# Optimization experiments

Hardware: AMD Instinct MI355X
Metric: run time of the kernel (lower is better)

Reference implementation:

```python
import jax, jax.numpy as jnp
import numpy as np

B, DIM, N, W, L = 8192, 100, 50, 256, 4  # paths, assets, timesteps, MLP width, n_layers
R = 0.05  # risk-free rate


def _mlp(x, W_in, b_in, W_h, b_h, W_out, b_out):
    # Net: Linear+ReLU, (L-1) hidden Linear+ReLU, final Linear (no activation)
    h = jax.nn.relu(x @ W_in + b_in)
    def body(h, wb):
        Wl, bl = wb
        return jax.nn.relu(h @ Wl + bl), None
    h, _ = jax.lax.scan(body, h, (W_h, b_h))
    return h @ W_out + b_out


def _init_net(key, n_in, n_out):
    ks = jax.random.split(key, 6)
    def lin(k, fi, fo):
        s = 1.0 / np.sqrt(fi)
        return jax.random.uniform(k, (fi, fo), jnp.float32, -s, s)
    W_in = lin(ks[0], n_in, W)
    b_in = jnp.zeros((W,), jnp.float32)
    W_h = jnp.stack([lin(jax.random.fold_in(ks[1], l), W, W) for l in range(L - 1)])
    b_h = jnp.zeros((L - 1, W), jnp.float32)
    W_out = lin(ks[2], W, n_out)
    b_out = jnp.zeros((n_out,), jnp.float32)
    return W_in, b_in, W_h, b_h, W_out, b_out


def setup_inputs() -> dict:
    key = jax.random.key(0)
    k_s0, k_dw, k_g, k_v = jax.random.split(key, 4)
    S0 = jax.random.uniform(k_s0, (B, DIM), jnp.float32, 0.5, 1.5)  # positive prices
    dW = jax.random.normal(k_dw, (N - 1, B, DIM), jnp.float32)  # unscaled increments
    timegrid = jnp.linspace(0.0, 1.0, N).astype(jnp.float32)
    # volatility matrix: rows of cholesky(cov) scaled by sigma_i
    cov = 0.9 * np.eye(DIM) + 0.1 * np.ones((DIM, DIM))
    C = np.linalg.cholesky(cov)
    sigma = 0.2 * np.ones(DIM)
    V = jnp.asarray(sigma[:, None] * C, jnp.float32)
    Wg_in, bg_in, Wg_h, bg_h, Wg_out, bg_out = _init_net(k_g, DIM + 1, DIM)
    Wv_in, bv_in, Wv_h, bv_h, Wv_out, bv_out = _init_net(k_v, DIM + 1, 1)
    return dict(S0=S0, dW=dW, timegrid=timegrid, volatility_mat=V,
                Wg_in=Wg_in, bg_in=bg_in, Wg_h=Wg_h, bg_h=bg_h, Wg_out=Wg_out, bg_out=bg_out,
                Wv_in=Wv_in, bv_in=bv_in, Wv_h=Wv_h, bv_h=bv_h, Wv_out=Wv_out, bv_out=bv_out)


def reference(S0, dW, timegrid, volatility_mat,
              Wg_in, bg_in, Wg_h, bg_h, Wg_out, bg_out,
              Wv_in, bv_in, Wv_h, bv_h, Wv_out, bv_out):
    r = jnp.float32(R)
    dt = timegrid[1:] - timegrid[:-1]                     # [N-1]
    dWs = jnp.sqrt(dt)[:, None, None] * dW                # sqrt(h)*randn, [N-1,B,DIM]
    bsz = S0.shape[0]

    inp0 = jnp.concatenate([jnp.full((bsz, 1), timegrid[0], S0.dtype), S0], axis=1)
    v0 = _mlp(inp0, Wv_in, bv_in, Wv_h, bv_h, Wv_out, bv_out)   # [B,1]

    def step(carry, xs):
        S_old, vOld, error = carry
        tp, tc, h, dWi = xs
        # S_old * (volatility_mat @ dW^T)^T == S_old * (dW @ V^T)
        vol = S_old * (dWi @ volatility_mat.T)                            # [B,DIM]
        inp_g = jnp.concatenate([jnp.full((bsz, 1), tp, S_old.dtype), S_old], axis=1)
        grad = _mlp(inp_g, Wg_in, bg_in, Wg_h, bg_h, Wg_out, bg_out)      # [B,DIM]
        stoch_int = jnp.sum(grad * vol, axis=1, keepdims=True)            # [B,1]
        S_new = S_old + r * S_old * h + vol
        inp_v = jnp.concatenate([jnp.full((bsz, 1), tc, S_new.dtype), S_new], axis=1)
        vNew = _mlp(inp_v, Wv_in, bv_in, Wv_h, bv_h, Wv_out, bv_out)      # [B,1]
        err_i = jax.lax.stop_gradient(vNew) - vOld * (1.0 + r * h) - stoch_int
        return (S_new, vNew, error + err_i ** 2), None

    init = (S0, v0, jnp.zeros_like(v0))
    (S_f, v_f, error), _ = jax.lax.scan(step, init, (timegrid[:-1], timegrid[1:], dt, dWs))
    return v_f, S_f, error
```

## Files before the change

### kernel.cpp

```cpp
#include <hip/hip_runtime.h>
#include <hip/hip_bf16.h>

#define DIMN 100
#define NPATH 8192
#define NT 50
#define HW 256
#define RRATE 0.05f

typedef __hip_bfloat16 bf16;
typedef _Float16 h16;
typedef __attribute__((ext_vector_type(8))) _Float16 h16x8;
typedef __attribute__((ext_vector_type(4))) _Float16 h16x4;
typedef __attribute__((ext_vector_type(4))) float f32x4;

__device__ __forceinline__ float ldin(const void* p, long i, int f32) {
    return f32 ? ((const float*)p)[i] : __bfloat162float(((const bf16*)p)[i]);
}

__global__ void probe_kernel(const void* tgp, int* flag) {
    if (threadIdx.x == 0 && blockIdx.x == 0) {
        const unsigned short* u = (const unsigned short*)tgp;
        *flag = (u[1] == 0) ? 1 : 0;
    }
}

__global__ void init_kernel(const void* S0, float* S_carry,
                            const void* V, float* Vt, const int* dflag) {
    const int f = *dflag;
    const long i = (long)blockIdx.x * blockDim.x + threadIdx.x;
    if (i < (long)NPATH * DIMN) S_carry[i] = ldin(S0, i, f);
    if (i < DIMN * DIMN) {
        const long d = i / DIMN, k = i % DIMN;
        Vt[k * DIMN + d] = ldin(V, d * DIMN + k, f);
    }
}

__global__ void pack_kernel(const void* Wg_in, const void* Wg_h, const void* Wg_out,
                            const void* Wv_in, const void* Wv_h,
                            h16* __restrict__ P, const int* __restrict__ dflag)
{
    const int f = *dflag;
    const long i = (long)blockIdx.x * blockDim.x + threadIdx.x;
    if (i >= 491520) return;
    long j; int NTk, kind; const void* src; long soff = 0;
    if (i < 32768)       { j = i;          NTk = 4; kind = 0; src = Wg_in; }
    else if (i < 229376) { long t = i - 32768;  j = t & 65535; NTk = 8; kind = 1; src = Wg_h;
                           soff = (long)(t >> 16) * 65536; }
    else if (i < 262144) { j = i - 229376; NTk = 8; kind = 2; src = Wg_out; }
    else if (i < 294912) { j = i - 262144; NTk = 4; kind = 0; src = Wv_in; }
    else                 { long t = i - 294912; j = t & 65535; NTk = 8; kind = 1; src = Wv_h;
                           soff = (long)(t >> 16) * 65536; }
    const int tile = (int)(j >> 9), lane = (int)((j >> 3) & 63), e = (int)(j & 7);
    const int tn = tile / NTk, tk = tile - tn * NTk;
    const int n = tn * 16 + (lane & 15);
    const int k = tk * 32 + (lane >> 4) * 8 + e;
    float v;
    if (kind == 0)      v = (k < 101) ? ldin(src, (long)k * 256 + n, f) : 0.f;
    else if (kind == 1) v = ldin(src, soff + (long)k * 256 + n, f);
    else                v = (n < 100) ? ldin(src, (long)k * 100 + n, f) : 0.f;
    P[i] = (h16)v;
}

template <bool A_RAW>
__global__ __launch_bounds__(256)
void gemm_kernel(const void* A, long aOff, int K,
                 const float* __restrict__ Bw, int N,
                 float* __restrict__ Cout, const int* __restrict__ dflag)
{
    const int f = *dflag;
    __shared__ float As[8][128];
    __shared__ float Bs[8][128];
    const int tid = threadIdx.x;
    const int tx = tid & 15, ty = tid >> 4;
    const long rowBase = (long)blockIdx.x * 128;
    const int colBase = blockIdx.y * 128;

    float acc[8][8];
#pragma unroll
    for (int i = 0; i < 8; i++)
#pragma unroll
        for (int j = 0; j < 8; j++) acc[i][j] = 0.f;

    for (int k0 = 0; k0 < K; k0 += 8) {
        {
            const int l = tid * 4;
            const int row = l >> 3;
            const int col = l & 7;
            const long abase = aOff + (rowBase + row) * (long)K + (k0 + col);
#pragma unroll
            for (int q = 0; q < 4; q++)
                As[col + q][row] = (k0 + col + q < K) ? ldin(A, abase + q, f) : 0.f;
        }
#pragma unroll
        for (int q = 0; q < 4; q++) {
            const int l = tid + 256 * q;
            const int kk = l >> 7, col = l & 127;
            const int gk = k0 + kk, gc = colBase + col;
            Bs[kk][col] = (gk < K && gc < N) ? Bw[(long)gk * N + gc] : 0.f;
        }
        __syncthreads();
#pragma unroll
        for (int kk = 0; kk < 8; kk++) {
            float a[8], b[8];
            const float4 a0 = *(const float4*)&As[kk][ty * 8];
            const float4 a1 = *(const float4*)&As[kk][ty * 8 + 4];
            const float4 b0 = *(const float4*)&Bs[kk][tx * 8];
            const float4 b1 = *(const float4*)&Bs[kk][tx * 8 + 4];
            a[0]=a0.x;a[1]=a0.y;a[2]=a0.z;a[3]=a0.w;a[4]=a1.x;a[5]=a1.y;a[6]=a1.z;a[7]=a1.w;
            b[0]=b0.x;b[1]=b0.y;b[2]=b0.z;b[3]=b0.w;b[4]=b1.x;b[5]=b1.y;b[6]=b1.z;b[7]=b1.w;
#pragma unroll
            for (int i = 0; i < 8; i++)
#pragma unroll
                for (int j = 0; j < 8; j++)
                    acc[i][j] += a[i] * b[j];
        }
        __syncthreads();
    }

#pragma unroll
    for (int i = 0; i < 8; i++) {
        const long row = rowBase + ty * 8 + i;
        const int colb = colBase + tx * 8;
        if (colb + 7 < N) {
            float4* cp = (float4*)(Cout + row * (long)N + colb);
            cp[0] = make_float4(acc[i][0], acc[i][1], acc[i][2], acc[i][3]);
            cp[1] = make_float4(acc[i][4], acc[i][5], acc[i][6], acc[i][7]);
        } else {
#pragma unroll
            for (int j = 0; j < 8; j++)
                if (colb + j < N) Cout[row * (long)N + colb + j] = acc[i][j];
        }
    }
}

__global__ __launch_bounds__(256)
void scan_chunk_kernel(float* __restrict__ S_carry, float* __restrict__ D,
                       const void* tgp, h16* __restrict__ Sh,
                       int t0, int Cg, void* outBase, h16* __restrict__ Shf,
                       int writeSf, const int* __restrict__ dflag)
{
    const int f = *dflag;
    const long idx = (long)blockIdx.x * blockDim.x + threadIdx.x;
    if (idx >= (long)NPATH * DIMN) return;
    const long b = idx / DIMN;
    const int d = (int)(idx - b * DIMN);
    float s = S_carry[idx];
    for (int lt = 0; lt < Cg; lt++) {
        const int t = t0 + lt;
        const float h = ldin(tgp, t + 1, f) - ldin(tgp, t, f);
        const long off = (long)lt * (NPATH * DIMN) + idx;
        const float vol = s * D[off] * sqrtf(h);
        const long shr = ((long)lt * NPATH + b) * 104;
        Sh[shr + 1 + d] = (h16)s;
        if (d == 0) Sh[shr] = (h16)ldin(tgp, t, f);
        if (d < 3) Sh[shr + 101 + d] = (h16)0.f;
        D[off] = vol;
        s = s + RRATE * s * h + vol;
    }
    S_carry[idx] = s;
    if (writeSf) {
        if (f) ((float*)outBase)[NPATH + idx] = s;
        else   ((bf16*)outBase)[NPATH + idx] = __float2bfloat16(s);
        Shf[b * 104 + 1 + d] = (h16)s;
        if (d == 0) Shf[b * 104] = (h16)ldin(tgp, NT - 1, f);
        if (d < 3) Shf[b * 104 + 101 + d] = (h16)0.f;
    }
}

template<int NTW>
__device__ __forceinline__ void init_acc(f32x4 acc[2][4], const float* __restrict__ bsrc,
                                         int nb16, int quad)
{
#pragma unroll
    for (int wt = 0; wt < NTW; wt++) {
        const f32x4 b4 = *(const f32x4*)(bsrc + nb16 + wt * 16 + quad * 4);
#pragma unroll
        for (int rt = 0; rt < 4; rt++) acc[wt][rt] = b4;
    }
}

template<int KP, int NTW>
__device__ __forceinline__ void layer_mfma(const h16* __restrict__ P,
                                           const h16 (*__restrict__ Hsp)[264],
                                           int tn0, int m, int quad, int lane,
                                           f32x4 acc[2][4])
{
    constexpr int NKT = KP >> 5;
    constexpr int TSTRIDE = NKT * 512;
    const h16* pw = P + (long)tn0 * TSTRIDE + lane * 8;
    h16x8 wf[2][NTW];
#pragma unroll
    for (int wt = 0; wt < NTW; wt++)
        wf[0][wt] = *(const h16x8*)(pw + wt * TSTRIDE);
#pragma unroll
    for (int wt = 0; wt < NTW; wt++)
        wf[1][wt] = *(const h16x8*)(pw + wt * TSTRIDE + 512);
#pragma unroll
    for (int kt = 0; kt < NKT; kt++) {
#pragma unroll
        for (int rt = 0; rt < 4; rt++) {
            const h16x8 hf = *(const h16x8*)&Hsp[rt * 16 + m][(kt << 5) + quad * 8];
#pragma unroll
            for (int wt = 0; wt < NTW; wt++)
                acc[wt][rt] = __builtin_amdgcn_mfma_f32_16x16x32_f16(
                    wf[kt & 1][wt], hf, acc[wt][rt], 0, 0, 0);
        }
        if (kt + 2 < NKT) {
#pragma unroll
            for (int wt = 0; wt < NTW; wt++)
                wf[kt & 1][wt] = *(const h16x8*)(pw + wt * TSTRIDE + (kt + 2) * 512);
        }
    }
}

template<int NTW>
__device__ __forceinline__ void writeback(f32x4 acc[2][4], h16 (*Hsp)[264],
                                          int nb16, int m, int quad)
{
    __syncthreads();
#pragma unroll
    for (int wt = 0; wt < NTW; wt++) {
        const int cb = nb16 + wt * 16 + quad * 4;
#pragma unroll
        for (int rt = 0; rt < 4; rt++) {
            const h16x4 pk = {(h16)fmaxf(acc[wt][rt][0], 0.f),
                              (h16)fmaxf(acc[wt][rt][1], 0.f),
                              (h16)fmaxf(acc[wt][rt][2], 0.f),
                              (h16)fmaxf(acc[wt][rt][3], 0.f)};
            *(h16x4*)&Hsp[rt * 16 + m][cb] = pk;
        }
    }
    __syncthreads();
}

template <bool GNET>
__global__ __launch_bounds__(512, 8)
void mlp16_kernel(const h16* __restrict__ Sh, const float* __restrict__ vol,
                  const h16* __restrict__ P0, const h16* __restrict__ Ph,
                  const h16* __restrict__ Pout,
                  const void* b_in, const void* b_h, const void* b_out,
                  const void* wv_out, const void* tgp, int t0,
                  float* __restrict__ outv, const int* __restrict__ dflag)
{
    const int f = *dflag;
    __shared__ __align__(16) h16 Hs[64][264];
    __shared__ __align__(16) float bias_s[4][256];
    __shared__ __align__(16) float ex_s[256];
    __shared__ float Ps[64][8];
    const int tid = threadIdx.x;
    const int w = tid >> 6, lane = tid & 63, quad = lane >> 4, m = lane & 15;
    const long row0 = (long)blockIdx.x * 64;

    {
        const int l = tid >> 7, c = (tid & 127) << 1;
        const void* bp = (l == 0) ? b_in : b_h;
        const long bo = (l == 0) ? 0 : (long)(l - 1) * 256;
        bias_s[l][c]     = ldin(bp, bo + c, f);
        bias_s[l][c + 1] = ldin(bp, bo + c + 1, f);
    }
    if (GNET) {
        if (tid < 128) ex_s[tid] = (tid < DIMN) ? ldin(b_out, tid, f) : 0.f;
    } else {
        if (tid < 256) ex_s[tid] = ldin(wv_out, tid, f);
    }

    {
        const int r = tid >> 3, j = tid & 7;
        const h16* src = Sh + (row0 + r) * 104;
        h16* dst = &Hs[r][0];
#pragma unroll
        for (int c = j; c < 16; c += 8) {
            if (c < 13)
                *(h16x8*)(dst + c * 8) = *(const h16x8*)(src + c * 8);
            else {
                const h16x8 z = {};
                *(h16x8*)(dst + c * 8) = z;
            }
        }
    }
    __syncthreads();

    f32x4 acc[2][4];

    init_acc<2>(acc, &bias_s[0][0], w * 32, quad);
    layer_mfma<128, 2>(P0, Hs, w * 2, m, quad, lane, acc);
    writeback<2>(acc, Hs, w * 32, m, quad);

    for (int li = 1; li < 4; li++) {
        init_acc<2>(acc, &bias_s[li][0], w * 32, quad);
        layer_mfma<256, 2>(Ph + (long)(li - 1) * 65536, Hs, w * 2, m, quad, lane, acc);
        writeback<2>(acc, Hs, w * 32, m, quad);
    }

    if (GNET) {
        init_acc<1>(acc, ex_s, w * 16, quad);
        layer_mfma<256, 1>(Pout, Hs, w, m, quad, lane, acc);

        float p[4] = {0.f, 0.f, 0.f, 0.f};
        const int cb = w * 16 + quad * 4;
        if (cb < DIMN) {
#pragma unroll
            for (int rt = 0; rt < 4; rt++) {
                const long r = row0 + rt * 16 + m;
                const float4 vv = *(const float4*)&vol[r * DIMN + cb];
                p[rt] += acc[0][rt][0] * vv.x + acc[0][rt][1] * vv.y
                       + acc[0][rt][2] * vv.z + acc[0][rt][3] * vv.w;
            }
        }
#pragma unroll
        for (int rt = 0; rt < 4; rt++) {
            float v = p[rt];
            v += __shfl_xor(v, 16);
            v += __shfl_xor(v, 32);
            if (quad == 0) Ps[rt * 16 + m][w] = v;
        }
        __syncthreads();
        if (tid < 64) {
            float s = 0.f;
#pragma unroll
            for (int q = 0; q < 8; q++) s += Ps[tid][q];
            outv[row0 + tid] = s;
        }
    } else {
        const int r = tid & 63, part = tid >> 6;
        float s = 0.f;
#pragma unroll
        for (int c = 0; c < 4; c++) {
            const h16x8 hv = *(const h16x8*)&Hs[r][part * 32 + c * 8];
#pragma unroll
            for (int q = 0; q < 8; q++)
                s += (float)hv[q] * ex_s[part * 32 + c * 8 + q];
        }
        Ps[r][part] = s;
        __syncthreads();
        if (tid < 64) {
            float s2 = 0.f;
#pragma unroll
            for (int q = 0; q < 8; q++) s2 += Ps[tid][q];
            outv[row0 + tid] = s2 + ldin(b_out, 0, f);
        }
    }
}

__global__ void final_kernel(const float* __restrict__ v_all, const float* __restrict__ stoch,
                             const void* tgp, void* out, const int* __restrict__ dflag)
{
    const int f = *dflag;
    const int b = blockIdx.x * blockDim.x + threadIdx.x;
    if (b >= NPATH) return;
    float err = 0.f;
    for (int i = 0; i < NT - 1; i++) {
        const float h = ldin(tgp, i + 1, f) - ldin(tgp, i, f);
        const float e = v_all[(i + 1) * NPATH + b] - v_all[i * NPATH + b] * (1.f + RRATE * h)
                        - stoch[i * NPATH + b];
        err += e * e;
    }
    const long eoff = (long)NPATH + (long)NPATH * DIMN;
    const float vf = v_all[(long)(NT - 1) * NPATH + b];
    if (f) {
        ((float*)out)[b] = vf;
        ((float*)out)[eoff + b] = err;
    } else {
        ((bf16*)out)[b] = __float2bfloat16(vf);
        ((bf16*)out)[eoff + b] = __float2bfloat16(err);
    }
}

static inline int imin(int a, int b) { return a < b ? a : b; }

extern "C" void kernel_launch(void* const* d_in, const int* in_sizes, int n_in,
                              void* d_out, int out_size, void* d_ws, size_t ws_size,
                              hipStream_t stream) {
    const void* S0    = d_in[0];
    const void* dW    = d_in[1];
    const void* tg    = d_in[2];
    const void* V     = d_in[3];
    const void* Wg_in = d_in[4];
    const void* bg_in = d_in[5];
    const void* Wg_h  = d_in[6];
    const void* bg_h  = d_in[7];
    const void* Wg_out= d_in[8];
    const void* bg_out= d_in[9];
    const void* Wv_in = d_in[10];
    const void* bv_in = d_in[11];
    const void* Wv_h  = d_in[12];
    const void* bv_h  = d_in[13];
    const void* Wv_out= d_in[14];
    const void* bv_out= d_in[15];

    const size_t SZ_SD  = (size_t)NPATH * DIMN * 4;
    const size_t SZ_SH  = (size_t)NPATH * 104 * 2;

    char* p = (char*)d_ws;
    auto carve = [&](size_t bytes) -> char* {
        char* r = p;
        p += (bytes + 255) & ~(size_t)255;
        return r;
    };
    int*   dflag     = (int*)carve(256);
    float* S_carry   = (float*)carve(SZ_SD);
    float* Vt        = (float*)carve((size_t)DIMN * DIMN * 4);
    float* v_all     = (float*)carve((size_t)NT * NPATH * 4);
    float* stoch_all = (float*)carve((size_t)(NT - 1) * NPATH * 4);
    h16*   Shf       = (h16*)carve(SZ_SH);
    h16*   Pk        = (h16*)carve((size_t)491520 * 2);
    const size_t fixed = (size_t)(p - (char*)d_ws);

    h16* Pg0   = Pk;
    h16* Pgh   = Pk + 32768;
    h16* Pgout = Pk + 229376;
    h16* Pv0   = Pk + 262144;
    h16* Pvh   = Pk + 294912;

    const size_t perC = SZ_SD + SZ_SH;
    size_t avail = (ws_size > fixed + 65536) ? (ws_size - fixed - 65536) : 0;
    int C = (int)(avail / perC);
    if (C < 1) C = 1;
    if (C > NT - 1) C = NT - 1;
    float* D_chunk = (float*)carve((size_t)C * SZ_SD);
    h16*   Sh      = (h16*)carve((size_t)C * SZ_SH);

    probe_kernel<<<dim3(1), dim3(64), 0, stream>>>(tg, dflag);
    init_kernel<<<dim3((NPATH * DIMN + 255) / 256), dim3(256), 0, stream>>>(S0, S_carry, V, Vt, dflag);
    pack_kernel<<<dim3(1920), dim3(256), 0, stream>>>(Wg_in, Wg_h, Wg_out, Wv_in, Wv_h, Pk, dflag);

    for (int t0 = 0; t0 < NT - 1; t0 += C) {
        const int Cg = imin(C, NT - 1 - t0);
        const int rows = Cg * NPATH;

        gemm_kernel<true><<<dim3(rows / 128, 1), 256, 0, stream>>>(
            dW, (long)t0 * NPATH * DIMN, DIMN, Vt, DIMN, D_chunk, dflag);

        scan_chunk_kernel<<<dim3((NPATH * DIMN + 255) / 256), 256, 0, stream>>>(
            S_carry, D_chunk, tg, Sh, t0, Cg, d_out, Shf,
            (t0 + Cg == NT - 1) ? 1 : 0, dflag);

        mlp16_kernel<true><<<dim3(rows / 64), 512, 0, stream>>>(
            Sh, D_chunk, Pg0, Pgh, Pgout, bg_in, bg_h, bg_out,
            nullptr, tg, t0, stoch_all + (long)t0 * NPATH, dflag);

        mlp16_kernel<false><<<dim3(rows / 64), 512, 0, stream>>>(
            Sh, nullptr, Pv0, Pvh, nullptr, bv_in, bv_h, bv_out,
            Wv_out, tg, t0, v_all + (long)t0 * NPATH, dflag);
    }

    mlp16_kernel<false><<<dim3(NPATH / 64), 512, 0, stream>>>(
        Shf, nullptr, Pv0, Pvh, nullptr, bv_in, bv_h, bv_out,
        Wv_out, tg, NT - 1, v_all + (long)(NT - 1) * NPATH, dflag);

    final_kernel<<<dim3(NPATH / 256), 256, 0, stream>>>(v_all, stoch_all, tg, d_out, dflag);
}
```

Baseline: 1.133 ms.

## Replace FP32 SIMT dW@V^T GEMM with split-fp16 MFMA GEMM

The correlated-increment GEMM (dW times V transpose) moves from a scalar FP32 shared-memory tiled kernel to an MFMA 16x16x32 fp16 kernel. To keep near-FP32 accuracy, both operands are split into high and low fp16 parts and combined with three MFMAs per tile. V is packed into the MFMA fragment layout inside the existing pack kernel rather than transposed in the init kernel. The goal is to cut the cost of this GEMM, which was a substantial share of the per-chunk work, at the price of extra MFMA work and some precision risk.

```diff
diff --git a/kernel.cpp b/kernel.cpp
--- a/kernel.cpp
+++ b/kernel.cpp
@@ -24,24 +24,32 @@
     }
 }
 
-__global__ void init_kernel(const void* S0, float* S_carry,
-                            const void* V, float* Vt, const int* dflag) {
+__global__ void init_kernel(const void* S0, float* S_carry, const int* dflag) {
     const int f = *dflag;
     const long i = (long)blockIdx.x * blockDim.x + threadIdx.x;
     if (i < (long)NPATH * DIMN) S_carry[i] = ldin(S0, i, f);
-    if (i < DIMN * DIMN) {
-        const long d = i / DIMN, k = i % DIMN;
-        Vt[k * DIMN + d] = ldin(V, d * DIMN + k, f);
-    }
 }
 
 __global__ void pack_kernel(const void* Wg_in, const void* Wg_h, const void* Wg_out,
-                            const void* Wv_in, const void* Wv_h,
+                            const void* Wv_in, const void* Wv_h, const void* Vmat,
                             h16* __restrict__ P, const int* __restrict__ dflag)
 {
     const int f = *dflag;
     const long i = (long)blockIdx.x * blockDim.x + threadIdx.x;
-    if (i >= 491520) return;
+    if (i >= 520192) return;
+    if (i >= 491520) {
+        const long j0 = i - 491520;
+        const int plane = (j0 >= 14336) ? 1 : 0;
+        const long j = plane ? (j0 - 14336) : j0;
+        const int tile = (int)(j >> 9), lane = (int)((j >> 3) & 63), e = (int)(j & 7);
+        const int tn = tile >> 2, tk = tile & 3;
+        const int d = tn * 16 + (lane & 15);
+        const int k = tk * 32 + (lane >> 4) * 8 + e;
+        float v = (d < DIMN && k < DIMN) ? ldin(Vmat, (long)d * DIMN + k, f) : 0.f;
+        const h16 hh = (h16)v;
+        P[i] = plane ? (h16)(v - (float)hh) : hh;
+        return;
+    }
     long j; int NTk, kind; const void* src; long soff = 0;
     if (i < 32768)       { j = i;          NTk = 4; kind = 0; src = Wg_in; }
     else if (i < 229376) { long t = i - 32768;  j = t & 65535; NTk = 8; kind = 1; src = Wg_h;
@@ -61,74 +69,82 @@
     P[i] = (h16)v;
 }
 
-template <bool A_RAW>
-__global__ __launch_bounds__(256)
-void gemm_kernel(const void* A, long aOff, int K,
-                 const float* __restrict__ Bw, int N,
-                 float* __restrict__ Cout, const int* __restrict__ dflag)
-{
-    const int f = *dflag;
-    __shared__ float As[8][128];
-    __shared__ float Bs[8][128];
+__global__ __launch_bounds__(256, 4)
+void gemm16_kernel(const void* dWp, long aOff, const h16* __restrict__ PH,
+                   const h16* __restrict__ PL, float* __restrict__ Dout,
+                   const int* __restrict__ dflag)
+{
+    const int f = *dflag;
+    __shared__ __align__(16) h16 AH[64][136];
+    __shared__ __align__(16) h16 AL[64][136];
     const int tid = threadIdx.x;
-    const int tx = tid & 15, ty = tid >> 4;
-    const long rowBase = (long)blockIdx.x * 128;
-    const int colBase = blockIdx.y * 128;
-
-    float acc[8][8];
-#pragma unroll
-    for (int i = 0; i < 8; i++)
-#pragma unroll
-        for (int j = 0; j < 8; j++) acc[i][j] = 0.f;
-
-    for (int k0 = 0; k0 < K; k0 += 8) {
-        {
-            const int l = tid * 4;
-            const int row = l >> 3;
-            const int col = l & 7;
-            const long abase = aOff + (rowBase + row) * (long)K + (k0 + col);
-#pragma unroll
-            for (int q = 0; q < 4; q++)
-                As[col + q][row] = (k0 + col + q < K) ? ldin(A, abase + q, f) : 0.f;
-        }
-#pragma unroll
-        for (int q = 0; q < 4; q++) {
-            const int l = tid + 256 * q;
-            const int kk = l >> 7, col = l & 127;
-            const int gk = k0 + kk, gc = colBase + col;
-            Bs[kk][col] = (gk < K && gc < N) ? Bw[(long)gk * N + gc] : 0.f;
-        }
-        __syncthreads();
-#pragma unroll
-        for (int kk = 0; kk < 8; kk++) {
-            float a[8], b[8];
-            const float4 a0 = *(const float4*)&As[kk][ty * 8];
-            const float4 a1 = *(const float4*)&As[kk][ty * 8 + 4];
-            const float4 b0 = *(const float4*)&Bs[kk][tx * 8];
-            const float4 b1 = *(const float4*)&Bs[kk][tx * 8 + 4];
-            a[0]=a0.x;a[1]=a0.y;a[2]=a0.z;a[3]=a0.w;a[4]=a1.x;a[5]=a1.y;a[6]=a1.z;a[7]=a1.w;
-            b[0]=b0.x;b[1]=b0.y;b[2]=b0.z;b[3]=b0.w;b[4]=b1.x;b[5]=b1.y;b[6]=b1.z;b[7]=b1.w;
-#pragma unroll
-            for (int i = 0; i < 8; i++)
-#pragma unroll
-                for (int j = 0; j < 8; j++)
-                    acc[i][j] += a[i] * b[j];
-        }
-        __syncthreads();
-    }
-
-#pragma unroll
-    for (int i = 0; i < 8; i++) {
-        const long row = rowBase + ty * 8 + i;
-        const int colb = colBase + tx * 8;
-        if (colb + 7 < N) {
-            float4* cp = (float4*)(Cout + row * (long)N + colb);
-            cp[0] = make_float4(acc[i][0], acc[i][1], acc[i][2], acc[i][3]);
-            cp[1] = make_float4(acc[i][4], acc[i][5], acc[i][6], acc[i][7]);
-        } else {
-#pragma unroll
-            for (int j = 0; j < 8; j++)
-                if (colb + j < N) Cout[row * (long)N + colb + j] = acc[i][j];
+    const int w = tid >> 6, lane = tid & 63, quad = lane >> 4, m = lane & 15;
+    const long row0 = (long)blockIdx.x * 64;
+
+    {
+        const long base = aOff + row0 * DIMN;
+#pragma unroll
+        for (int q = 0; q < 25; q++) {
+            const int i = tid + 256 * q;
+            const unsigned r = (unsigned)i / 100u;
+            const int c = i - (int)r * 100;
+            const float x = ldin(dWp, base + i, f);
+            const h16 h = (h16)x;
+            AH[r][c] = h;
+            AL[r][c] = (h16)(x - (float)h);
+        }
+        const int r = tid >> 2, p = tid & 3;
+#pragma unroll
+        for (int j = 0; j < 7; j++) {
+            AH[r][100 + p * 7 + j] = (h16)0.f;
+            AL[r][100 + p * 7 + j] = (h16)0.f;
+        }
+    }
+    __syncthreads();
+
+    f32x4 acc[2][4];
+#pragma unroll
+    for (int wt = 0; wt < 2; wt++)
+#pragma unroll
+        for (int rt = 0; rt < 4; rt++) acc[wt][rt] = (f32x4){0.f, 0.f, 0.f, 0.f};
+
+    const int tn0 = w * 2;
+    const int tn1c = (tn0 + 1 > 6) ? 6 : tn0 + 1;
+    const h16* pwh[2] = { PH + (long)tn0 * 2048 + lane * 8,
+                          PH + (long)tn1c * 2048 + lane * 8 };
+    const h16* pwl[2] = { PL + (long)tn0 * 2048 + lane * 8,
+                          PL + (long)tn1c * 2048 + lane * 8 };
+#pragma unroll
+    for (int kt = 0; kt < 4; kt++) {
+        h16x8 wh[2], wl[2];
+#pragma unroll
+        for (int wt = 0; wt < 2; wt++) {
+            wh[wt] = *(const h16x8*)(pwh[wt] + kt * 512);
+            wl[wt] = *(const h16x8*)(pwl[wt] + kt * 512);
+        }
+#pragma unroll
+        for (int rt = 0; rt < 4; rt++) {
+            const h16x8 ah = *(const h16x8*)&AH[rt * 16 + m][kt * 32 + quad * 8];
+            const h16x8 al = *(const h16x8*)&AL[rt * 16 + m][kt * 32 + quad * 8];
+#pragma unroll
+            for (int wt = 0; wt < 2; wt++) {
+                acc[wt][rt] = __builtin_amdgcn_mfma_f32_16x16x32_f16(wl[wt], ah, acc[wt][rt], 0, 0, 0);
+                acc[wt][rt] = __builtin_amdgcn_mfma_f32_16x16x32_f16(wh[wt], al, acc[wt][rt], 0, 0, 0);
+                acc[wt][rt] = __builtin_amdgcn_mfma_f32_16x16x32_f16(wh[wt], ah, acc[wt][rt], 0, 0, 0);
+            }
+        }
+    }
+
+#pragma unroll
+    for (int wt = 0; wt < 2; wt++) {
+        const int cb = (tn0 + wt) * 16 + quad * 4;
+        if (cb < DIMN) {
+#pragma unroll
+            for (int rt = 0; rt < 4; rt++) {
+                float4* dp = (float4*)(Dout + (row0 + rt * 16 + m) * (long)DIMN + cb);
+                *dp = make_float4(acc[wt][rt][0], acc[wt][rt][1],
+                                  acc[wt][rt][2], acc[wt][rt][3]);
+            }
         }
     }
 }
@@ -399,11 +415,10 @@
     };
     int*   dflag     = (int*)carve(256);
     float* S_carry   = (float*)carve(SZ_SD);
-    float* Vt        = (float*)carve((size_t)DIMN * DIMN * 4);
     float* v_all     = (float*)carve((size_t)NT * NPATH * 4);
     float* stoch_all = (float*)carve((size_t)(NT - 1) * NPATH * 4);
     h16*   Shf       = (h16*)carve(SZ_SH);
-    h16*   Pk        = (h16*)carve((size_t)491520 * 2);
+    h16*   Pk        = (h16*)carve((size_t)520192 * 2);
     const size_t fixed = (size_t)(p - (char*)d_ws);
 
     h16* Pg0   = Pk;
@@ -411,6 +426,8 @@
     h16* Pgout = Pk + 229376;
     h16* Pv0   = Pk + 262144;
     h16* Pvh   = Pk + 294912;
+    h16* PvtH  = Pk + 491520;
+    h16* PvtL  = Pk + 505856;
 
     const size_t perC = SZ_SD + SZ_SH;
     size_t avail = (ws_size > fixed + 65536) ? (ws_size - fixed - 65536) : 0;
@@ -421,15 +438,15 @@
     h16*   Sh      = (h16*)carve((size_t)C * SZ_SH);
 
     probe_kernel<<<dim3(1), dim3(64), 0, stream>>>(tg, dflag);
-    init_kernel<<<dim3((NPATH * DIMN + 255) / 256), dim3(256), 0, stream>>>(S0, S_carry, V, Vt, dflag);
-    pack_kernel<<<dim3(1920), dim3(256), 0, stream>>>(Wg_in, Wg_h, Wg_out, Wv_in, Wv_h, Pk, dflag);
+    init_kernel<<<dim3((NPATH * DIMN + 255) / 256), dim3(256), 0, stream>>>(S0, S_carry, dflag);
+    pack_kernel<<<dim3(2032), dim3(256), 0, stream>>>(Wg_in, Wg_h, Wg_out, Wv_in, Wv_h, V, Pk, dflag);
 
     for (int t0 = 0; t0 < NT - 1; t0 += C) {
         const int Cg = imin(C, NT - 1 - t0);
         const int rows = Cg * NPATH;
 
-        gemm_kernel<true><<<dim3(rows / 128, 1), 256, 0, stream>>>(
-            dW, (long)t0 * NPATH * DIMN, DIMN, Vt, DIMN, D_chunk, dflag);
+        gemm16_kernel<<<dim3(rows / 64), 256, 0, stream>>>(
+            dW, (long)t0 * NPATH * DIMN, PvtH, PvtL, D_chunk, dflag);
 
         scan_chunk_kernel<<<dim3((NPATH * DIMN + 255) / 256), 256, 0, stream>>>(
             S_carry, D_chunk, tg, Sh, t0, Cg, d_out, Shf,
```

Measured after the change: 981.0 us. 1.15x faster.
